# Optimization experiments

Hardware: AMD Instinct MI355X
Metric: run time of the kernel (lower is better)

The kernel has to match this reference:

```python
import jax, jax.numpy as jnp
import numpy as np

B, H, N, F, P = 32, 64, 2048, 1, 24
U = N * F  # LSTM units (must equal N for carry shapes to be valid)


def setup_inputs() -> dict:
    key = jax.random.key(0)
    ks = jax.random.split(key, 6)
    s_in = 1.0 / np.sqrt(N)
    s_rec = 1.0 / np.sqrt(U)
    return {
        "inputs": jax.random.normal(ks[0], (B, H, N, F), dtype=jnp.float32),
        "pca_components": jax.random.normal(ks[1], (N, N * F), dtype=jnp.float32) * (1.0 / np.sqrt(N * F)),
        "pca_mean": jax.random.normal(ks[2], (N * F,), dtype=jnp.float32) * 0.1,
        "kernel": jax.random.normal(ks[3], (N, 4 * U), dtype=jnp.float32) * s_in,
        "recurrent_kernel": jax.random.normal(ks[4], (U, 4 * U), dtype=jnp.float32) * s_rec,
        "bias": jnp.zeros((4 * U,), dtype=jnp.float32).at[U:2 * U].set(1.0),  # unit forget bias
    }


def _cell(h, c, x, kernel, recurrent_kernel, bias):
    # Keras LSTMCell gate math: z split as [i, f, g, o]
    z = x @ kernel + h @ recurrent_kernel + bias  # (B, 4U)
    i, f, g, o = jnp.split(z, 4, axis=-1)
    i = jax.nn.sigmoid(i)
    f = jax.nn.sigmoid(f)
    g = jnp.tanh(g)
    o = jax.nn.sigmoid(o)
    c_new = f * c + i * g
    h_new = o * jnp.tanh(c_new)
    return h_new, c_new


def reference(inputs, pca_components, pca_mean, kernel, recurrent_kernel, bias):
    b, h_steps, n, f = inputs.shape
    # PCA transform applied to every timestep at once: (x - mean) @ components.T
    flat = inputs.reshape(b, h_steps, n * f)  # (B, H, N*F)
    xs = (flat - pca_mean) @ pca_components.T  # (B, H, N)
    xs_t = jnp.swapaxes(xs, 0, 1)  # (H, B, N) for scan over time

    h0 = jnp.zeros((b, U), dtype=inputs.dtype)
    c0 = jnp.zeros((b, U), dtype=inputs.dtype)

    def enc_step(carry, x):
        h, c = carry
        h, c = _cell(h, c, x, kernel, recurrent_kernel, bias)
        return (h, c), None

    (h, c), _ = jax.lax.scan(enc_step, (h0, c0), xs_t)

    def dec_step(carry, _):
        h, c = carry
        # input to the cell is the previous output (memory == h)
        h, c = _cell(h, c, h, kernel, recurrent_kernel, bias)
        return (h, c), h

    (_, _), preds = jax.lax.scan(dec_step, (h, c), None, length=P)  # (P, B, U)
    return jnp.swapaxes(preds, 0, 1)  # (B, P, U)
```

## Files before the change

kernel.cpp:

```cpp
#include <hip/hip_runtime.h>
#include <math.h>


typedef unsigned short US;
typedef __attribute__((ext_vector_type(8))) _Float16 f16x8;
typedef __attribute__((ext_vector_type(4))) float f32x4;

typedef __attribute__((address_space(3))) unsigned int as3_uint;
typedef __attribute__((address_space(1))) unsigned int as1_uint;

#define MFMA16(a, b, c) __builtin_amdgcn_mfma_f32_16x16x32_f16(a, b, c, 0, 0, 0)

__device__ __forceinline__ US f2h(float x) {
  _Float16 h = (_Float16)x;
  return __builtin_bit_cast(US, h);
}
__device__ __forceinline__ float h2f(US u) {
  return (float)__builtin_bit_cast(_Float16, u);
}

__device__ __forceinline__ void gl_lds16(const US* g, US* l) {
  __builtin_amdgcn_global_load_lds((const as1_uint*)g, (as3_uint*)l, 16, 0, 0);
}

__global__ __launch_bounds__(256) void split16_kernel(
    const float* __restrict__ in, US* __restrict__ hi, US* __restrict__ lo, int n4)
{
  int i = blockIdx.x * 256 + threadIdx.x;
  if (i >= n4) return;
  float4 v = reinterpret_cast<const float4*>(in)[i];
  US h0 = f2h(v.x), h1 = f2h(v.y), h2 = f2h(v.z), h3 = f2h(v.w);
  reinterpret_cast<ushort4*>(hi)[i] = make_ushort4(h0, h1, h2, h3);
  reinterpret_cast<ushort4*>(lo)[i] =
      make_ushort4(f2h(v.x - h2f(h0)), f2h(v.y - h2f(h1)),
                   f2h(v.z - h2f(h2)), f2h(v.w - h2f(h3)));
}

__global__ __launch_bounds__(256) void cvt16_kernel(
    const float* __restrict__ in, US* __restrict__ o16, int n4)
{
  int i = blockIdx.x * 256 + threadIdx.x;
  if (i >= n4) return;
  float4 v = reinterpret_cast<const float4*>(in)[i];
  reinterpret_cast<ushort4*>(o16)[i] =
      make_ushort4(f2h(v.x), f2h(v.y), f2h(v.z), f2h(v.w));
}

__global__ void zero_kernel(float* __restrict__ c, US* __restrict__ h0)
{
  int i = blockIdx.x * 256 + threadIdx.x;
  c[i] = 0.f; h0[i] = 0;
}

__global__ __launch_bounds__(256) void mproj_kernel(
    const float* __restrict__ mean, const float* __restrict__ comp,
    float* __restrict__ mproj)
{
  int j = blockIdx.x;
  const float* row = comp + (size_t)j * 2048;
  float s = 0.f;
  for (int k = threadIdx.x; k < 2048; k += 256) s += mean[k] * row[k];
  __shared__ float ss[4];
  #pragma unroll
  for (int o = 32; o > 0; o >>= 1) s += __shfl_down(s, o, 64);
  if ((threadIdx.x & 63) == 0) ss[threadIdx.x >> 6] = s;
  __syncthreads();
  if (threadIdx.x == 0) mproj[j] = ss[0] + ss[1] + ss[2] + ss[3];
}

__global__ __launch_bounds__(256) void build_weights(
    const float* __restrict__ Rsrc, const float* __restrict__ Ksrc,
    US* __restrict__ KT, US* __restrict__ tR, US* __restrict__ tS)
{
  __shared__ float tileR[64][68];
  __shared__ float tileK[64][68];
  const int ub = blockIdx.x >> 5;
  const int kb = blockIdx.x & 31;
  const int u0 = ub * 16, k0 = kb * 64;
  const int j0 = ub * 64;
  const int jg0 = ub * 4, kc0 = kb * 2;
  const int tid = threadIdx.x;

  const int g = tid >> 6, r2 = (tid >> 2) & 15, c4 = tid & 3;
  #pragma unroll
  for (int rr = 0; rr < 4; ++rr) {
    int row = rr * 16 + r2;
    size_t off = (size_t)(k0 + row) * 8192 + g * 2048 + u0 + c4 * 4;
    float4 v = *reinterpret_cast<const float4*>(Rsrc + off);
    float4 w = *reinterpret_cast<const float4*>(Ksrc + off);
    tileR[4 * (c4 * 4 + 0) + g][row] = v.x;
    tileR[4 * (c4 * 4 + 1) + g][row] = v.y;
    tileR[4 * (c4 * 4 + 2) + g][row] = v.z;
    tileR[4 * (c4 * 4 + 3) + g][row] = v.w;
    tileK[4 * (c4 * 4 + 0) + g][row] = w.x;
    tileK[4 * (c4 * 4 + 1) + g][row] = w.y;
    tileK[4 * (c4 * 4 + 2) + g][row] = w.z;
    tileK[4 * (c4 * 4 + 3) + g][row] = w.w;
  }
  __syncthreads();

  {
    const int klw = tid & 63, jl0 = tid >> 6;
    #pragma unroll
    for (int r = 0; r < 16; ++r) {
      int jl = r * 4 + jl0;
      KT[(size_t)(j0 + jl) * 2048 + (size_t)(k0 + klw)] = f2h(tileK[jl][klw]);
    }
  }
  #pragma unroll
  for (int it = 0; it < 2; ++it) {
    int idx = it * 256 + tid;
    int l = idx & 63, kcl = (idx >> 6) & 1, jgl = idx >> 7;
    int jloc = jgl * 16 + (l & 15);
    int kl = kcl * 32 + (l >> 4) * 8;
    size_t base = (((size_t)(jg0 + jgl) * 64 + (kc0 + kcl)) * 64 + l) * 8;
    unsigned int hr[4], hs[4];
    #pragma unroll
    for (int q = 0; q < 4; ++q) {
      float r0 = tileR[jloc][kl + 2 * q],     r1 = tileR[jloc][kl + 2 * q + 1];
      float k0v = tileK[jloc][kl + 2 * q],    k1v = tileK[jloc][kl + 2 * q + 1];
      hr[q] = (unsigned int)f2h(r0) | ((unsigned int)f2h(r1) << 16);
      hs[q] = (unsigned int)f2h(r0 + k0v) | ((unsigned int)f2h(r1 + k1v) << 16);
    }
    *reinterpret_cast<uint4*>(tR + base) = make_uint4(hr[0], hr[1], hr[2], hr[3]);
    *reinterpret_cast<uint4*>(tS + base) = make_uint4(hs[0], hs[1], hs[2], hs[3]);
  }
}

template<int NT, int EPI>
__global__ __launch_bounds__(256, 2) void gemm128h(
    const US* __restrict__ Ah, const US* __restrict__ Al,
    const US* __restrict__ B, const float* __restrict__ mproj,
    US* __restrict__ out0, US* __restrict__ out1,
    int MB, int ldo)
{
  constexpr int BN = NT * 32;
  __shared__ US sAh[128 * 64], sAl[128 * 64];
  __shared__ US sB[BN * 64];
  const int tid = threadIdx.x;
  const int w = tid >> 6, l = tid & 63;
  const int l16 = l & 15, lq = l >> 4;
  const int cpx = gridDim.x >> 3;
  const int swz = (blockIdx.x & 7) * cpx + (blockIdx.x >> 3);
  const int bm = swz % MB, bn = swz / MB;
  const int wm = w & 1, wn = w >> 1;
  const int AR0 = bm * 128, BR0 = bn * BN;

  f32x4 acc[4][NT];
  #pragma unroll
  for (int i = 0; i < 4; ++i)
    #pragma unroll
    for (int j = 0; j < NT; ++j) acc[i][j] = {0.f, 0.f, 0.f, 0.f};

  for (int k0 = 0; k0 < 2048; k0 += 64) {
    {
      #pragma unroll
      for (int i = 0; i < 4; ++i) {
        int c = (w * 4 + i) * 64 + l;
        int row = c >> 3, kc = c & 7;
        size_t go = (size_t)(AR0 + row) * 2048 + (k0 + ((kc ^ (row & 7)) << 3));
        gl_lds16(Ah + go, sAh + (w * 4 + i) * 512);
        gl_lds16(Al + go, sAl + (w * 4 + i) * 512);
      }
      constexpr int IPW = BN >> 5;
      #pragma unroll
      for (int i = 0; i < IPW; ++i) {
        int c = (w * IPW + i) * 64 + l;
        int row = c >> 3, kc = c & 7;
        size_t go = (size_t)(BR0 + row) * 2048 + (k0 + ((kc ^ (row & 7)) << 3));
        gl_lds16(B + go, sB + (w * IPW + i) * 512);
      }
    }
    __syncthreads();
    #pragma unroll
    for (int ks = 0; ks < 2; ++ks) {
      const int kb = ks * 64 + lq * 16;
      f16x8 ah[4], al[4], bb[NT];
      #pragma unroll
      for (int mt = 0; mt < 4; ++mt) {
        int r = wm * 64 + mt * 16 + l16;
        int off = r * 64 + ((kb ^ ((r & 7) << 4)) >> 1);
        ah[mt] = *reinterpret_cast<const f16x8*>(sAh + off);
        al[mt] = *reinterpret_cast<const f16x8*>(sAl + off);
      }
      #pragma unroll
      for (int nt = 0; nt < NT; ++nt) {
        int r = wn * (BN / 2) + nt * 16 + l16;
        int off = r * 64 + ((kb ^ ((r & 7) << 4)) >> 1);
        bb[nt] = *reinterpret_cast<const f16x8*>(sB + off);
      }
      #pragma unroll
      for (int mt = 0; mt < 4; ++mt)
        #pragma unroll
        for (int nt = 0; nt < NT; ++nt) {
          acc[mt][nt] = MFMA16(ah[mt], bb[nt], acc[mt][nt]);
          acc[mt][nt] = MFMA16(al[mt], bb[nt], acc[mt][nt]);
        }
    }
    __syncthreads();
  }

  #pragma unroll
  for (int mt = 0; mt < 4; ++mt)
    #pragma unroll
    for (int nt = 0; nt < NT; ++nt) {
      int j = BR0 + wn * (BN / 2) + nt * 16 + l16;
      float mp = (EPI == 0) ? mproj[j] : 0.f;
      #pragma unroll
      for (int r = 0; r < 4; ++r) {
        int m = AR0 + wm * 64 + mt * 16 + lq * 4 + r;
        float v = acc[mt][nt][r] - mp;
        if constexpr (EPI == 0) {
          int t = m & 63, b = m >> 6;
          size_t o = (size_t)(t * 32 + b) * ldo + j;
          US hv = f2h(v);
          out0[o] = hv;
          out1[o] = f2h(v - h2f(hv));
        } else {
          out0[(size_t)m * ldo + j] = f2h(v);
        }
      }
    }
}

__global__ __launch_bounds__(512, 4) void lstm_step16(
    const US* __restrict__ hf,
    const US* __restrict__ wf,
    const US* __restrict__ zx,
    const float* __restrict__ bias, float* __restrict__ cst,
    US* __restrict__ ho,
    float* __restrict__ pred, int p)
{
  __shared__ float red[7][64][17];
  __shared__ float zbuf[32][33];
  const int tid = threadIdx.x;
  const int kq = tid >> 6, l = tid & 63;
  const int b = blockIdx.x;
  const int l16 = l & 15, lq = l >> 4;

  const US* wp0 = wf + (((size_t)(2 * b) * 64 + kq * 8) * 64 + l) * 8;
  const US* wp1 = wp0 + (size_t)64 * 64 * 8;
  const US* ah  = hf + (((size_t)kq * 16) * 64 + l) * 8;

  f32x4 acc00 = {0.f,0.f,0.f,0.f}, acc01 = {0.f,0.f,0.f,0.f};
  f32x4 acc10 = {0.f,0.f,0.f,0.f}, acc11 = {0.f,0.f,0.f,0.f};
  #pragma unroll
  for (int c = 0; c < 8; ++c) {
    f16x8 w0 = *reinterpret_cast<const f16x8*>(wp0 + c * 512);
    f16x8 w1 = *reinterpret_cast<const f16x8*>(wp1 + c * 512);
    f16x8 a0 = *reinterpret_cast<const f16x8*>(ah + c * 1024);
    f16x8 a1 = *reinterpret_cast<const f16x8*>(ah + c * 1024 + 512);
    acc00 = MFMA16(a0, w0, acc00);
    acc10 = MFMA16(a1, w0, acc10);
    acc01 = MFMA16(a0, w1, acc01);
    acc11 = MFMA16(a1, w1, acc11);
  }

  if (kq > 0) {
    #pragma unroll
    for (int r = 0; r < 4; ++r) {
      red[kq - 1][l][r]      = acc00[r];
      red[kq - 1][l][r + 4]  = acc01[r];
      red[kq - 1][l][r + 8]  = acc10[r];
      red[kq - 1][l][r + 12] = acc11[r];
    }
  }
  __syncthreads();
  if (kq == 0) {
    #pragma unroll
    for (int q = 0; q < 7; ++q)
      #pragma unroll
      for (int r = 0; r < 4; ++r) {
        acc00[r] += red[q][l][r];
        acc01[r] += red[q][l][r + 4];
        acc10[r] += red[q][l][r + 8];
        acc11[r] += red[q][l][r + 12];
      }
    #pragma unroll
    for (int r = 0; r < 4; ++r) {
      zbuf[lq * 4 + r][l16]           = acc00[r];
      zbuf[lq * 4 + r][16 + l16]      = acc01[r];
      zbuf[16 + lq * 4 + r][l16]      = acc10[r];
      zbuf[16 + lq * 4 + r][16 + l16] = acc11[r];
    }
  }
  __syncthreads();

  if (tid < 256) {
    int m = tid >> 3, ul = tid & 7;
    int u = b * 8 + ul;
    float zi = zbuf[m][ul * 4 + 0] + bias[u];
    float zf = zbuf[m][ul * 4 + 1] + bias[u + 2048];
    float zg = zbuf[m][ul * 4 + 2] + bias[u + 4096];
    float zo = zbuf[m][ul * 4 + 3] + bias[u + 6144];
    if (zx) {
      ushort4 zr = *reinterpret_cast<const ushort4*>(
          zx + (size_t)m * 8192 + (size_t)u * 4);
      zi += h2f(zr.x); zf += h2f(zr.y); zg += h2f(zr.z); zo += h2f(zr.w);
    }
    float gi = 1.f / (1.f + expf(-zi));
    float gf = 1.f / (1.f + expf(-zf));
    float gg = tanhf(zg);
    float go = 1.f / (1.f + expf(-zo));
    float cn = gf * cst[m * 2048 + u] + gi * gg;
    float hn = go * tanhf(cn);
    cst[m * 2048 + u] = cn;
    int kc = u >> 5, mh = m >> 4;
    int lw = ((u >> 3) & 3) * 16 + (m & 15);
    int e = u & 7;
    ho[(((size_t)kc * 2 + mh) * 64 + lw) * 8 + e] = f2h(hn);
    if (p >= 0) pred[(size_t)(m * 24 + p) * 2048 + u] = hn;
  }
}

extern "C" void kernel_launch(void* const* d_in, const int* in_sizes, int n_in,
                              void* d_out, int out_size, void* d_ws, size_t ws_size,
                              hipStream_t stream)
{
  const float* inputs = (const float*)d_in[0];
  const float* comp   = (const float*)d_in[1];
  const float* mean   = (const float*)d_in[2];
  const float* Kmat   = (const float*)d_in[3];
  const float* Rmat   = (const float*)d_in[4];
  const float* bias   = (const float*)d_in[5];
  float* out = (float*)d_out;

  const size_t MiB = 1024 * 1024;
  char* base = (char*)d_ws;
  US* zx16     = (US*)(base);
  US* KT       = (US*)(base + 32 * MiB);
  US* RTf      = (US*)(base + 64 * MiB);
  US* WSTf     = (US*)(base + 96 * MiB);
  US* flat_hi  = (US*)(base + 128 * MiB);
  US* flat_lo  = (US*)(base + 136 * MiB);
  US* comp16   = (US*)(base + 144 * MiB);
  US* xs_hi    = (US*)(base + 152 * MiB);
  US* xs_lo    = (US*)(base + 160 * MiB);
  char* Mz = base + 168 * MiB;
  float* mproj = (float*)(Mz);
  float* cbuf  = (float*)(Mz + 64 * 1024);
  US* hh[2];
  hh[0] = (US*)(Mz + 320 * 1024);
  hh[1] = (US*)(Mz + 448 * 1024);

  split16_kernel<<<4096, 256, 0, stream>>>(inputs, flat_hi, flat_lo, 1048576);
  cvt16_kernel<<<4096, 256, 0, stream>>>(comp, comp16, 1048576);
  mproj_kernel<<<2048, 256, 0, stream>>>(mean, comp, mproj);
  zero_kernel<<<256, 256, 0, stream>>>(cbuf, hh[0]);
  build_weights<<<4096, 256, 0, stream>>>(Rmat, Kmat, KT, RTf, WSTf);

  gemm128h<2, 0><<<512, 256, 0, stream>>>(flat_hi, flat_lo, comp16,
                                          mproj, xs_hi, xs_lo, 16, 2048);
  gemm128h<4, 1><<<1024, 256, 0, stream>>>(xs_hi, xs_lo, KT,
                                           nullptr, zx16, nullptr, 16, 8192);

  for (int s = 0; s < 64; ++s) {
    int par = s & 1;
    lstm_step16<<<256, 512, 0, stream>>>(hh[par], RTf,
                                         zx16 + (size_t)s * 32 * 8192,
                                         bias, cbuf, hh[1 - par],
                                         out, -1);
  }
  for (int s = 64; s < 88; ++s) {
    int par = s & 1;
    lstm_step16<<<256, 512, 0, stream>>>(hh[par], WSTf,
                                         nullptr,
                                         bias, cbuf, hh[1 - par],
                                         out, s - 64);
  }
}
```

Measured before the change: 955.3 us.

## Drop hi/lo fp16 split in PCA and input GEMMs; flatten LSTM reduction

Removes the hi/lo fp16 error-compensation split for the inputs and the PCA output. Both precompute GEMMs now run single fp16 MFMAs with one A tile, halving A-side loads, LDS use and MFMA count. The LSTM step kernel also changes its cross-wave reduction: all 8 waves write partial sums to shared memory and 256 threads each sum 8 values, instead of wave 0 accumulating serially. This trades accuracy in the input projections for less precompute work.

```diff
diff --git a/kernel.cpp b/kernel.cpp
--- a/kernel.cpp
+++ b/kernel.cpp
@@ -21,19 +21,6 @@
 
 __device__ __forceinline__ void gl_lds16(const US* g, US* l) {
   __builtin_amdgcn_global_load_lds((const as1_uint*)g, (as3_uint*)l, 16, 0, 0);
-}
-
-__global__ __launch_bounds__(256) void split16_kernel(
-    const float* __restrict__ in, US* __restrict__ hi, US* __restrict__ lo, int n4)
-{
-  int i = blockIdx.x * 256 + threadIdx.x;
-  if (i >= n4) return;
-  float4 v = reinterpret_cast<const float4*>(in)[i];
-  US h0 = f2h(v.x), h1 = f2h(v.y), h2 = f2h(v.z), h3 = f2h(v.w);
-  reinterpret_cast<ushort4*>(hi)[i] = make_ushort4(h0, h1, h2, h3);
-  reinterpret_cast<ushort4*>(lo)[i] =
-      make_ushort4(f2h(v.x - h2f(h0)), f2h(v.y - h2f(h1)),
-                   f2h(v.z - h2f(h2)), f2h(v.w - h2f(h3)));
 }
 
 __global__ __launch_bounds__(256) void cvt16_kernel(
@@ -129,13 +116,12 @@
 
 template<int NT, int EPI>
 __global__ __launch_bounds__(256, 2) void gemm128h(
-    const US* __restrict__ Ah, const US* __restrict__ Al,
-    const US* __restrict__ B, const float* __restrict__ mproj,
-    US* __restrict__ out0, US* __restrict__ out1,
-    int MB, int ldo)
+    const US* __restrict__ A, const US* __restrict__ B,
+    const float* __restrict__ mproj,
+    US* __restrict__ out0, int MB, int ldo)
 {
   constexpr int BN = NT * 32;
-  __shared__ US sAh[128 * 64], sAl[128 * 64];
+  __shared__ US sA[128 * 64];
   __shared__ US sB[BN * 64];
   const int tid = threadIdx.x;
   const int w = tid >> 6, l = tid & 63;
@@ -159,8 +145,7 @@
         int c = (w * 4 + i) * 64 + l;
         int row = c >> 3, kc = c & 7;
         size_t go = (size_t)(AR0 + row) * 2048 + (k0 + ((kc ^ (row & 7)) << 3));
-        gl_lds16(Ah + go, sAh + (w * 4 + i) * 512);
-        gl_lds16(Al + go, sAl + (w * 4 + i) * 512);
+        gl_lds16(A + go, sA + (w * 4 + i) * 512);
       }
       constexpr int IPW = BN >> 5;
       #pragma unroll
@@ -175,13 +160,12 @@
     #pragma unroll
     for (int ks = 0; ks < 2; ++ks) {
       const int kb = ks * 64 + lq * 16;
-      f16x8 ah[4], al[4], bb[NT];
+      f16x8 ah[4], bb[NT];
       #pragma unroll
       for (int mt = 0; mt < 4; ++mt) {
         int r = wm * 64 + mt * 16 + l16;
         int off = r * 64 + ((kb ^ ((r & 7) << 4)) >> 1);
-        ah[mt] = *reinterpret_cast<const f16x8*>(sAh + off);
-        al[mt] = *reinterpret_cast<const f16x8*>(sAl + off);
+        ah[mt] = *reinterpret_cast<const f16x8*>(sA + off);
       }
       #pragma unroll
       for (int nt = 0; nt < NT; ++nt) {
@@ -192,10 +176,8 @@
       #pragma unroll
       for (int mt = 0; mt < 4; ++mt)
         #pragma unroll
-        for (int nt = 0; nt < NT; ++nt) {
+        for (int nt = 0; nt < NT; ++nt)
           acc[mt][nt] = MFMA16(ah[mt], bb[nt], acc[mt][nt]);
-          acc[mt][nt] = MFMA16(al[mt], bb[nt], acc[mt][nt]);
-        }
     }
     __syncthreads();
   }
@@ -211,11 +193,8 @@
         int m = AR0 + wm * 64 + mt * 16 + lq * 4 + r;
         float v = acc[mt][nt][r] - mp;
         if constexpr (EPI == 0) {
-          int t = m & 63, b = m >> 6;
-          size_t o = (size_t)(t * 32 + b) * ldo + j;
-          US hv = f2h(v);
-          out0[o] = hv;
-          out1[o] = f2h(v - h2f(hv));
+          int t = m & 63, bb_ = m >> 6;
+          out0[(size_t)(t * 32 + bb_) * ldo + j] = f2h(v);
         } else {
           out0[(size_t)m * ldo + j] = f2h(v);
         }
@@ -231,8 +210,7 @@
     US* __restrict__ ho,
     float* __restrict__ pred, int p)
 {
-  __shared__ float red[7][64][17];
-  __shared__ float zbuf[32][33];
+  __shared__ float red[8][32][33];
   const int tid = threadIdx.x;
   const int kq = tid >> 6, l = tid & 63;
   const int b = blockIdx.x;
@@ -256,52 +234,35 @@
     acc11 = MFMA16(a1, w1, acc11);
   }
 
-  if (kq > 0) {
-    #pragma unroll
-    for (int r = 0; r < 4; ++r) {
-      red[kq - 1][l][r]      = acc00[r];
-      red[kq - 1][l][r + 4]  = acc01[r];
-      red[kq - 1][l][r + 8]  = acc10[r];
-      red[kq - 1][l][r + 12] = acc11[r];
-    }
-  }
-  __syncthreads();
-  if (kq == 0) {
-    #pragma unroll
-    for (int q = 0; q < 7; ++q)
-      #pragma unroll
-      for (int r = 0; r < 4; ++r) {
-        acc00[r] += red[q][l][r];
-        acc01[r] += red[q][l][r + 4];
-        acc10[r] += red[q][l][r + 8];
-        acc11[r] += red[q][l][r + 12];
-      }
-    #pragma unroll
-    for (int r = 0; r < 4; ++r) {
-      zbuf[lq * 4 + r][l16]           = acc00[r];
-      zbuf[lq * 4 + r][16 + l16]      = acc01[r];
-      zbuf[16 + lq * 4 + r][l16]      = acc10[r];
-      zbuf[16 + lq * 4 + r][16 + l16] = acc11[r];
-    }
+  #pragma unroll
+  for (int r = 0; r < 4; ++r) {
+    red[kq][l16][lq * 4 + r]           = acc00[r];
+    red[kq][16 + l16][lq * 4 + r]      = acc01[r];
+    red[kq][l16][16 + lq * 4 + r]      = acc10[r];
+    red[kq][16 + l16][16 + lq * 4 + r] = acc11[r];
   }
   __syncthreads();
 
   if (tid < 256) {
     int m = tid >> 3, ul = tid & 7;
     int u = b * 8 + ul;
-    float zi = zbuf[m][ul * 4 + 0] + bias[u];
-    float zf = zbuf[m][ul * 4 + 1] + bias[u + 2048];
-    float zg = zbuf[m][ul * 4 + 2] + bias[u + 4096];
-    float zo = zbuf[m][ul * 4 + 3] + bias[u + 6144];
+    float z[4];
+    #pragma unroll
+    for (int g = 0; g < 4; ++g) {
+      float s = bias[u + g * 2048];
+      #pragma unroll
+      for (int q = 0; q < 8; ++q) s += red[q][ul * 4 + g][m];
+      z[g] = s;
+    }
     if (zx) {
       ushort4 zr = *reinterpret_cast<const ushort4*>(
           zx + (size_t)m * 8192 + (size_t)u * 4);
-      zi += h2f(zr.x); zf += h2f(zr.y); zg += h2f(zr.z); zo += h2f(zr.w);
-    }
-    float gi = 1.f / (1.f + expf(-zi));
-    float gf = 1.f / (1.f + expf(-zf));
-    float gg = tanhf(zg);
-    float go = 1.f / (1.f + expf(-zo));
+      z[0] += h2f(zr.x); z[1] += h2f(zr.y); z[2] += h2f(zr.z); z[3] += h2f(zr.w);
+    }
+    float gi = 1.f / (1.f + expf(-z[0]));
+    float gf = 1.f / (1.f + expf(-z[1]));
+    float gg = tanhf(z[2]);
+    float go = 1.f / (1.f + expf(-z[3]));
     float cn = gf * cst[m * 2048 + u] + gi * gg;
     float hn = go * tanhf(cn);
     cst[m * 2048 + u] = cn;
@@ -331,28 +292,26 @@
   US* KT       = (US*)(base + 32 * MiB);
   US* RTf      = (US*)(base + 64 * MiB);
   US* WSTf     = (US*)(base + 96 * MiB);
-  US* flat_hi  = (US*)(base + 128 * MiB);
-  US* flat_lo  = (US*)(base + 136 * MiB);
-  US* comp16   = (US*)(base + 144 * MiB);
-  US* xs_hi    = (US*)(base + 152 * MiB);
-  US* xs_lo    = (US*)(base + 160 * MiB);
-  char* Mz = base + 168 * MiB;
+  US* flat16   = (US*)(base + 128 * MiB);
+  US* comp16   = (US*)(base + 136 * MiB);
+  US* xs16     = (US*)(base + 144 * MiB);
+  char* Mz = base + 152 * MiB;
   float* mproj = (float*)(Mz);
   float* cbuf  = (float*)(Mz + 64 * 1024);
   US* hh[2];
   hh[0] = (US*)(Mz + 320 * 1024);
   hh[1] = (US*)(Mz + 448 * 1024);
 
-  split16_kernel<<<4096, 256, 0, stream>>>(inputs, flat_hi, flat_lo, 1048576);
+  cvt16_kernel<<<4096, 256, 0, stream>>>(inputs, flat16, 1048576);
   cvt16_kernel<<<4096, 256, 0, stream>>>(comp, comp16, 1048576);
   mproj_kernel<<<2048, 256, 0, stream>>>(mean, comp, mproj);
   zero_kernel<<<256, 256, 0, stream>>>(cbuf, hh[0]);
   build_weights<<<4096, 256, 0, stream>>>(Rmat, Kmat, KT, RTf, WSTf);
 
-  gemm128h<2, 0><<<512, 256, 0, stream>>>(flat_hi, flat_lo, comp16,
-                                          mproj, xs_hi, xs_lo, 16, 2048);
-  gemm128h<4, 1><<<1024, 256, 0, stream>>>(xs_hi, xs_lo, KT,
-                                           nullptr, zx16, nullptr, 16, 8192);
+  gemm128h<2, 0><<<512, 256, 0, stream>>>(flat16, comp16, mproj,
+                                          xs16, 16, 2048);
+  gemm128h<4, 1><<<1024, 256, 0, stream>>>(xs16, KT, nullptr,
+                                           zx16, 16, 8192);
 
   for (int s = 0; s < 64; ++s) {
     int par = s & 1;
```

Measured after the change: 806.9 us. 1.18x faster.
